# Performance work log

Measured on AMD Instinct MI355X. Metric: run time of the kernel, lower is better.

Reference implementation:

```python
import jax, jax.numpy as jnp
import numpy as np

B, S, D, H = 4, 2048, 1024, 16
HD = D // H


def setup_inputs() -> dict:
    key = jax.random.key(0)
    ks = jax.random.split(key, 12)
    def lin(k):
        return jax.random.normal(k, (D, D), dtype=jnp.float32) * 0.02
    return {
        "query": jax.random.normal(ks[0], (B, S, D), dtype=jnp.float32),
        "key": jax.random.normal(ks[1], (B, S, D), dtype=jnp.float32),
        "value": jax.random.normal(ks[2], (B, S, D), dtype=jnp.float32),
        "Wq": lin(ks[3]), "bq": jnp.zeros((D,), jnp.float32),
        "Wk": lin(ks[4]), "bk": jnp.zeros((D,), jnp.float32),
        "Wv": lin(ks[5]), "bv": jnp.zeros((D,), jnp.float32),
        "Wo": lin(ks[6]), "bo": jnp.zeros((D,), jnp.float32),
        "pad_mask": jnp.ones((B, S), dtype=jnp.int32),
    }


def reference(query, key, value, Wq, bq, Wk, bk, Wv, bv, Wo, bo, pad_mask):
    # torch nn.Linear convention: y = x @ W.T + b
    Q = query @ Wq.T + bq   # [B,Sq,D]
    K = key @ Wk.T + bk     # [B,Sk,D]
    V = value @ Wv.T + bv
    Sq, Sk = Q.shape[1], K.shape[1]
    Q = Q.reshape(B, Sq, H, HD).transpose(0, 2, 1, 3)  # [B,H,Sq,hd]
    K = K.reshape(B, Sk, H, HD).transpose(0, 2, 1, 3)
    V = V.reshape(B, Sk, H, HD).transpose(0, 2, 1, 3)
    scores = jnp.einsum('bhqd,bhkd->bhqk', Q, K) / jnp.sqrt(jnp.float32(HD))
    # causal (lookahead) mask
    causal = jnp.tril(jnp.ones((Sq, Sk), dtype=bool))
    scores = jnp.where(causal[None, None], scores, -jnp.inf)
    # pad mask broadcast [B,1,Sq,1]
    pm = (pad_mask[:, None, :, None] != 0)
    scores = jnp.where(pm, scores, -jnp.inf)
    attn = jax.nn.softmax(scores, axis=-1)
    out = jnp.einsum('bhqk,bhkd->bhqd', attn, V)  # [B,H,Sq,hd]
    out = out.transpose(0, 2, 1, 3).reshape(B, Sq, D)
    return out @ Wo.T + bo
```

## Files before the change

kernel.cpp:

```cpp
#include <hip/hip_runtime.h>
#include <hip/hip_bf16.h>
#include <stdint.h>

typedef __attribute__((ext_vector_type(8))) short bf16x8;
typedef __attribute__((ext_vector_type(4))) float f32x4;

#define HD 64
#define NH 16
#define SEQ 2048
#define DM 1024

#define GLDS16(gp, lp)                                                      \
    __builtin_amdgcn_global_load_lds(                                       \
        (const __attribute__((address_space(1))) void*)(gp),                \
        (__attribute__((address_space(3))) void*)(lp), 16, 0, 0)

__device__ __forceinline__ unsigned pk2(float lo, float hi) {
    union { unsigned u; __hip_bfloat16 h[2]; } w;
    w.h[0] = __float2bfloat16(lo);
    w.h[1] = __float2bfloat16(hi);
    return w.u;
}

__device__ inline bf16x8 cvt8(const float* __restrict__ p) {
    float4 a = *(const float4*)p;
    float4 b = *(const float4*)(p + 4);
    union { bf16x8 v; __hip_bfloat16 e[8]; } u;
    u.e[0] = __float2bfloat16(a.x); u.e[1] = __float2bfloat16(a.y);
    u.e[2] = __float2bfloat16(a.z); u.e[3] = __float2bfloat16(a.w);
    u.e[4] = __float2bfloat16(b.x); u.e[5] = __float2bfloat16(b.y);
    u.e[6] = __float2bfloat16(b.z); u.e[7] = __float2bfloat16(b.w);
    return u.v;
}

__global__ __launch_bounds__(256)
void cvtw(const float* __restrict__ a, const float* __restrict__ b,
          const float* __restrict__ c, const float* __restrict__ d,
          __hip_bfloat16* __restrict__ o)
{
    int g = blockIdx.x * 256 + threadIdx.x;
    int t = g * 4;
    const float* src;
    switch (t >> 20) {
        case 0: src = a; break;
        case 1: src = b; break;
        case 2: src = c; break;
        default: src = d; break;
    }
    float4 v = *(const float4*)(src + (t & 0xFFFFF));
    union { ushort4 u; __hip_bfloat16 e[4]; } w;
    w.e[0] = __float2bfloat16(v.x); w.e[1] = __float2bfloat16(v.y);
    w.e[2] = __float2bfloat16(v.z); w.e[3] = __float2bfloat16(v.w);
    *(ushort4*)(o + t) = w.u;
}

__device__ __forceinline__ bf16x8 ldfrag_f32(const char* base, int row, int quad) {
    f32x4 a = *(const f32x4*)(base + (size_t)row * 128 + (((2 * quad)     ^ (row & 7)) * 16));
    f32x4 b = *(const f32x4*)(base + (size_t)row * 128 + (((2 * quad + 1) ^ (row & 7)) * 16));
    union { bf16x8 v; unsigned u[4]; } w;
    w.u[0] = pk2(a[0], a[1]); w.u[1] = pk2(a[2], a[3]);
    w.u[2] = pk2(b[0], b[1]); w.u[3] = pk2(b[2], b[3]);
    return w.v;
}

__global__ __launch_bounds__(256, 4)
void qkvgemm(const float* __restrict__ Xq, const float* __restrict__ Xk,
             const float* __restrict__ Xv,
             const __hip_bfloat16* __restrict__ wb,
             const float* __restrict__ bq, const float* __restrict__ bk,
             const float* __restrict__ bv,
             __hip_bfloat16* __restrict__ Qh, __hip_bfloat16* __restrict__ Kh,
             __hip_bfloat16* __restrict__ Vt, float scaleQ)
{
    __shared__ alignas(16) float As[128 * 32];
    __shared__ alignas(16) __hip_bfloat16 Bs[128 * 32];

    const int tid  = threadIdx.x;
    const int lane = tid & 63;
    const int wv   = tid >> 6;
    const int quad = lane >> 4;
    const int l15  = lane & 15;
    const int wm   = (wv >> 1) * 64;
    const int wn   = (wv & 1) * 64;
    const int z    = blockIdx.z;

    const float* X = (z == 0) ? Xq : (z == 1) ? Xk : Xv;
    const __hip_bfloat16* W = wb + (size_t)z * (1024 * 1024);
    const float* bias = (z == 0) ? bq : (z == 1) ? bk : bv;

    int lin = blockIdx.y * 8 + blockIdx.x;
    const int bx = lin >> 6;
    const int by = ((lin & 7) << 3) | ((lin >> 3) & 7);
    const int m0 = by * 128;
    const int n0 = bx * 128;

    f32x4 acc[4][4] = {};

    for (int k0 = 0; k0 < 1024; k0 += 32) {
        #pragma unroll
        for (int it = 0; it < 4; ++it) {
            int g = tid + it * 256;
            int row = g >> 3, cl = (g & 7) ^ (row & 7);
            GLDS16(&X[(size_t)(m0 + row) * 1024 + k0 + cl * 4],
                   (char*)As + (size_t)g * 16);
        }
        #pragma unroll
        for (int it = 0; it < 2; ++it) {
            int c = tid + it * 256;
            int row = c >> 2, cg = c & 3;
            GLDS16(&W[(size_t)(n0 + row) * 1024 + k0 + cg * 8],
                   (char*)Bs + (size_t)c * 16);
        }
        __syncthreads();

        bf16x8 af[4], bfr[4];
        #pragma unroll
        for (int i = 0; i < 4; ++i)
            af[i] = ldfrag_f32((const char*)As, wm + i * 16 + l15, quad);
        #pragma unroll
        for (int j = 0; j < 4; ++j)
            bfr[j] = *(const bf16x8*)(&Bs[(wn + j * 16 + l15) * 32 + quad * 8]);

        #pragma unroll
        for (int i = 0; i < 4; ++i)
            #pragma unroll
            for (int j = 0; j < 4; ++j)
                acc[i][j] = __builtin_amdgcn_mfma_f32_16x16x32_bf16(
                    af[i], bfr[j], acc[i][j], 0, 0, 0);
        __syncthreads();
    }

    const float scale = (z == 0) ? scaleQ : 1.0f;
    #pragma unroll
    for (int j = 0; j < 4; ++j) {
        int n = n0 + wn + j * 16 + l15;
        float bv2 = bias[n];
        int h = n >> 6, hd = n & 63;
        #pragma unroll
        for (int i = 0; i < 4; ++i) {
            int mb = m0 + wm + i * 16 + quad * 4;
            if (z < 2) {
                __hip_bfloat16* Y = (z == 0) ? Qh : Kh;
                #pragma unroll
                for (int r = 0; r < 4; ++r) {
                    int m = mb + r;
                    int b = m >> 11, s = m & 2047;
                    Y[((size_t)(b * NH + h) * SEQ + s) * HD + hd] =
                        __float2bfloat16((acc[i][j][r] + bv2) * scale);
                }
            } else {
                int b = mb >> 11, s = mb & 2047;
                union { ushort4 u; __hip_bfloat16 e[4]; } w;
                #pragma unroll
                for (int r = 0; r < 4; ++r)
                    w.e[r] = __float2bfloat16(acc[i][j][r] + bv2);
                *(ushort4*)(&Vt[((size_t)(b * NH + h) * HD + hd) * SEQ + s]) = w.u;
            }
        }
    }
}

__global__ __launch_bounds__(256)
void ogemm(const __hip_bfloat16* __restrict__ X,
           const __hip_bfloat16* __restrict__ Wb,
           const float* __restrict__ bias,
           float* __restrict__ Y,
           int M, int N, int K)
{
    __shared__ alignas(16) __hip_bfloat16 As[128 * 32];
    __shared__ alignas(16) __hip_bfloat16 Bs[128 * 32];

    const int tid  = threadIdx.x;
    const int lane = tid & 63;
    const int wv   = tid >> 6;
    const int quad = lane >> 4;
    const int l15  = lane & 15;
    const int wm   = (wv >> 1) * 64;
    const int wn   = (wv & 1) * 64;

    int lin = blockIdx.y * 8 + blockIdx.x;
    const int bx = lin >> 6;
    const int by = ((lin & 7) << 3) | ((lin >> 3) & 7);
    const int m0 = by * 128;
    const int n0 = bx * 128;

    f32x4 acc[4][4] = {};

    for (int k0 = 0; k0 < K; k0 += 32) {
        #pragma unroll
        for (int it = 0; it < 2; ++it) {
            int c = tid + it * 256;
            int row = c >> 2, cg = c & 3;
            GLDS16(&X[(size_t)(m0 + row) * K + k0 + cg * 8],
                   (char*)As + (size_t)c * 16);
            GLDS16(&Wb[(size_t)(n0 + row) * K + k0 + cg * 8],
                   (char*)Bs + (size_t)c * 16);
        }
        __syncthreads();

        bf16x8 af[4], bfr[4];
        #pragma unroll
        for (int i = 0; i < 4; ++i)
            af[i] = *(const bf16x8*)(&As[(wm + i * 16 + l15) * 32 + quad * 8]);
        #pragma unroll
        for (int j = 0; j < 4; ++j)
            bfr[j] = *(const bf16x8*)(&Bs[(wn + j * 16 + l15) * 32 + quad * 8]);

        #pragma unroll
        for (int i = 0; i < 4; ++i)
            #pragma unroll
            for (int j = 0; j < 4; ++j)
                acc[i][j] = __builtin_amdgcn_mfma_f32_16x16x32_bf16(
                    af[i], bfr[j], acc[i][j], 0, 0, 0);
        __syncthreads();
    }

    #pragma unroll
    for (int j = 0; j < 4; ++j) {
        int n = n0 + wn + j * 16 + l15;
        float bv = bias[n];
        #pragma unroll
        for (int i = 0; i < 4; ++i) {
            int mb = m0 + wm + i * 16 + quad * 4;
            #pragma unroll
            for (int r = 0; r < 4; ++r)
                Y[(size_t)(mb + r) * N + n] = acc[i][j][r] + bv;
        }
    }
}

__device__ __forceinline__ void swap16(unsigned& a, unsigned& b) {
    asm("v_permlane16_swap_b32 %0, %1" : "+v"(a), "+v"(b));
}

__device__ __forceinline__ void attn_tile(
    const bf16x8 (&aqs)[2], f32x4 (&os)[4], f32x4& o5,
    const __hip_bfloat16* __restrict__ K_, const __hip_bfloat16* __restrict__ V_,
    const bf16x8 ones, int kv0, int qabs, bool diag,
    int quad, int l15, int sw, int qp)
{
    f32x4 sv[4];
    __builtin_amdgcn_s_setprio(1);
    #pragma unroll
    for (int jk = 0; jk < 4; ++jk) {
        f32x4 s = {};
        #pragma unroll
        for (int ks = 0; ks < 2; ++ks) {
            bf16x8 kf = *(const bf16x8*)(
                &K_[(jk * 16 + l15) * 64 + (((ks * 4 + quad) ^ sw) * 8)]);
            s = __builtin_amdgcn_mfma_f32_16x16x32_bf16(kf, aqs[ks], s, 0, 0, 0);
        }
        sv[jk] = s;
    }
    __builtin_amdgcn_s_setprio(0);
    unsigned P[4][2];
    #pragma unroll
    for (int jk = 0; jk < 4; ++jk) {
        int kvb = kv0 + jk * 16 + quad * 4;
        #pragma unroll
        for (int h = 0; h < 2; ++h) {
            float e0 = __builtin_amdgcn_exp2f(sv[jk][2 * h]);
            float e1 = __builtin_amdgcn_exp2f(sv[jk][2 * h + 1]);
            if (diag) {
                e0 = (kvb + 2 * h     <= qabs) ? e0 : 0.f;
                e1 = (kvb + 2 * h + 1 <= qabs) ? e1 : 0.f;
            }
            P[jk][h] = pk2(e0, e1);
        }
    }
    swap16(P[0][0], P[1][0]);
    swap16(P[0][1], P[1][1]);
    swap16(P[2][0], P[3][0]);
    swap16(P[2][1], P[3][1]);
    union { bf16x8 v; unsigned u[4]; } fa0, fa1;
    fa0.u[0] = P[0][0]; fa0.u[1] = P[0][1]; fa0.u[2] = P[1][0]; fa0.u[3] = P[1][1];
    fa1.u[0] = P[2][0]; fa1.u[1] = P[2][1]; fa1.u[2] = P[3][0]; fa1.u[3] = P[3][1];
    __builtin_amdgcn_s_setprio(1);
    #pragma unroll
    for (int jn = 0; jn < 4; ++jn) {
        bf16x8 vb0 = *(const bf16x8*)(
            &V_[(jn * 16 + l15) * 64 + ((qp ^ sw) * 8)]);
        bf16x8 vb1 = *(const bf16x8*)(
            &V_[(jn * 16 + l15) * 64 + (((4 + qp) ^ sw) * 8)]);
        os[jn] = __builtin_amdgcn_mfma_f32_16x16x32_bf16(fa0.v, vb0, os[jn], 0, 0, 0);
        os[jn] = __builtin_amdgcn_mfma_f32_16x16x32_bf16(fa1.v, vb1, os[jn], 0, 0, 0);
    }
    o5 = __builtin_amdgcn_mfma_f32_16x16x32_bf16(fa0.v, ones, o5, 0, 0, 0);
    o5 = __builtin_amdgcn_mfma_f32_16x16x32_bf16(fa1.v, ones, o5, 0, 0, 0);
    __builtin_amdgcn_s_setprio(0);
}

__global__ __launch_bounds__(256, 4)
void attn(const __hip_bfloat16* __restrict__ Qh,
          const __hip_bfloat16* __restrict__ Kh,
          const __hip_bfloat16* __restrict__ Vt,
          __hip_bfloat16* __restrict__ O)
{
    __shared__ alignas(16) __hip_bfloat16 Ks[2][64 * 64];
    __shared__ alignas(16) __hip_bfloat16 VsT[2][64 * 64];

    const int tid  = threadIdx.x;
    const int lane = tid & 63;
    const int wv   = tid >> 6;
    const int quad = lane >> 4;
    const int l15  = lane & 15;
    const int bh   = blockIdx.y;
    const int b    = bh >> 4;
    const int h    = bh & 15;
    const int p    = blockIdx.x;
    const int sa   = p;
    const int sb   = 31 - p;
    const int sw   = l15 & 7;
    const int qp   = ((quad & 1) << 1) | (quad >> 1);

    const __hip_bfloat16* Qp  = Qh + (size_t)bh * SEQ * HD;
    const __hip_bfloat16* Kp  = Kh + (size_t)bh * SEQ * HD;
    const __hip_bfloat16* Vtp = Vt + (size_t)bh * HD * SEQ;

    union { bf16x8 v; short e[8]; } onesu;
    #pragma unroll
    for (int i = 0; i < 8; ++i) onesu.e[i] = (short)0x3F80;
    const bf16x8 ones = onesu.v;

    bf16x8 aq[2][2];
    #pragma unroll
    for (int s = 0; s < 2; ++s) {
        int qb = (s ? sb : sa) * 64;
        #pragma unroll
        for (int ks = 0; ks < 2; ++ks)
            aq[s][ks] = *(const bf16x8*)(
                &Qp[(size_t)(qb + wv * 16 + l15) * HD + ks * 32 + quad * 8]);
    }

    f32x4 o[2][4] = {};
    f32x4 o5[2]   = {};

    const int srow = tid >> 3;
    const int scg  = (tid & 7) ^ (srow & 7);
    const __hip_bfloat16* kSrc = Kp + (size_t)srow * HD + scg * 8;
    const __hip_bfloat16* vSrc = Vtp + (size_t)srow * SEQ + scg * 8;
    char* kDst0 = (char*)Ks[0]  + tid * 16;
    char* vDst0 = (char*)VsT[0] + tid * 16;

    auto STAGE = [&](int bufi, int kv0) {
        size_t kadv = (size_t)kv0 * HD;
        int boff = bufi * 8192;
        GLDS16(kSrc + kadv,           kDst0 + boff);
        GLDS16(kSrc + kadv + 32 * HD, kDst0 + boff + 4096);
        GLDS16(vSrc + kv0,            vDst0 + boff);
        GLDS16(vSrc + kv0 + 32 * SEQ, vDst0 + boff + 4096);
    };

    const int nit = sa + sb + 2;

    STAGE(0, 0);

    for (int i = 0; i < nit; ++i) {
        __syncthreads();

        int ni = i + 1;
        if (ni < nit) {
            int t2 = (ni <= sb) ? ni : ni - sb - 1;
            STAGE(ni & 1, t2 * 64);
        }

        const int cb    = i & 1;
        const bool isB  = (i <= sb);
        const int t     = isB ? i : i - sb - 1;
        const int strip = isB ? sb : sa;
        const int kv0   = t * 64;
        const bool diag = (t == strip);
        const int qabs  = strip * 64 + wv * 16 + l15;

        const __hip_bfloat16* K_ = Ks[cb];
        const __hip_bfloat16* V_ = VsT[cb];

        if (isB)
            attn_tile(aq[1], o[1], o5[1], K_, V_, ones, kv0, qabs, diag, quad, l15, sw, qp);
        else
            attn_tile(aq[0], o[0], o5[0], K_, V_, ones, kv0, qabs, diag, quad, l15, sw, qp);
    }

    #pragma unroll
    for (int s = 0; s < 2; ++s) {
        int strip = s ? sb : sa;
        float inv[4];
        #pragma unroll
        for (int r = 0; r < 4; ++r)
            inv[r] = 1.0f / o5[s][r];
        #pragma unroll
        for (int jn = 0; jn < 4; ++jn) {
            #pragma unroll
            for (int r = 0; r < 4; ++r) {
                int q = strip * 64 + wv * 16 + quad * 4 + r;
                O[((size_t)(b * SEQ + q)) * DM + h * HD + jn * 16 + l15] =
                    __float2bfloat16(o[s][jn][r] * inv[r]);
            }
        }
    }
}

extern "C" void kernel_launch(void* const* d_in, const int* in_sizes, int n_in,
                              void* d_out, int out_size, void* d_ws, size_t ws_size,
                              hipStream_t stream)
{
    const float* query = (const float*)d_in[0];
    const float* key_  = (const float*)d_in[1];
    const float* value = (const float*)d_in[2];
    const float* Wq = (const float*)d_in[3];
    const float* bq = (const float*)d_in[4];
    const float* Wk = (const float*)d_in[5];
    const float* bk = (const float*)d_in[6];
    const float* Wv = (const float*)d_in[7];
    const float* bv = (const float*)d_in[8];
    const float* Wo = (const float*)d_in[9];
    const float* bo = (const float*)d_in[10];

    const size_t WSZ = (size_t)1024 * 1024;
    const size_t MAT = (size_t)8192 * 1024;
    __hip_bfloat16* wb = (__hip_bfloat16*)d_ws;
    __hip_bfloat16* Qh = wb + 4 * WSZ;
    __hip_bfloat16* Kh = Qh + MAT;
    __hip_bfloat16* Vt = Kh + MAT;
    __hip_bfloat16* Oa = Vt + MAT;
    float* out = (float*)d_out;

    const float SC = 0.18033688f;

    dim3 bb(256);
    cvtw<<<4096, bb, 0, stream>>>(Wq, Wk, Wv, Wo, wb);
    qkvgemm<<<dim3(8, 64, 3), bb, 0, stream>>>(query, key_, value, wb,
                                               bq, bk, bv, Qh, Kh, Vt, SC);
    attn<<<dim3(16, 64), bb, 0, stream>>>(Qh, Kh, Vt, Oa);
    ogemm<<<dim3(8, 64), bb, 0, stream>>>(Oa, wb + 3 * WSZ, bo, out, 8192, 1024, 1024);
}
```

Measured before the change: 350.6 us.

## Double-buffer LDS tiles in QKV and output projection GEMMs

Both projection GEMMs now use two LDS buffers. The next K-tile's global-to-LDS loads are issued right after the barrier, so they run while MFMA work proceeds on the current tile. This also removes one of the two barriers per iteration, and ogemm gets a launch-bounds occupancy hint of 4 blocks. The cost is doubled LDS per block, which may reduce resident blocks for qkvgemm; if the compiler conservatively waits on the LDS-DMA loads before the LDS reads, the overlap will not happen.

```diff
diff --git a/kernel.cpp b/kernel.cpp
--- a/kernel.cpp
+++ b/kernel.cpp
@@ -20,17 +20,6 @@
     w.h[0] = __float2bfloat16(lo);
     w.h[1] = __float2bfloat16(hi);
     return w.u;
-}
-
-__device__ inline bf16x8 cvt8(const float* __restrict__ p) {
-    float4 a = *(const float4*)p;
-    float4 b = *(const float4*)(p + 4);
-    union { bf16x8 v; __hip_bfloat16 e[8]; } u;
-    u.e[0] = __float2bfloat16(a.x); u.e[1] = __float2bfloat16(a.y);
-    u.e[2] = __float2bfloat16(a.z); u.e[3] = __float2bfloat16(a.w);
-    u.e[4] = __float2bfloat16(b.x); u.e[5] = __float2bfloat16(b.y);
-    u.e[6] = __float2bfloat16(b.z); u.e[7] = __float2bfloat16(b.w);
-    return u.v;
 }
 
 __global__ __launch_bounds__(256)
@@ -72,8 +61,8 @@
              __hip_bfloat16* __restrict__ Qh, __hip_bfloat16* __restrict__ Kh,
              __hip_bfloat16* __restrict__ Vt, float scaleQ)
 {
-    __shared__ alignas(16) float As[128 * 32];
-    __shared__ alignas(16) __hip_bfloat16 Bs[128 * 32];
+    __shared__ alignas(16) float As[2][128 * 32];
+    __shared__ alignas(16) __hip_bfloat16 Bs[2][128 * 32];
 
     const int tid  = threadIdx.x;
     const int lane = tid & 63;
@@ -96,30 +85,38 @@
 
     f32x4 acc[4][4] = {};
 
-    for (int k0 = 0; k0 < 1024; k0 += 32) {
+    auto STAGE = [&](int bufi, int k0) {
         #pragma unroll
         for (int it = 0; it < 4; ++it) {
             int g = tid + it * 256;
             int row = g >> 3, cl = (g & 7) ^ (row & 7);
             GLDS16(&X[(size_t)(m0 + row) * 1024 + k0 + cl * 4],
-                   (char*)As + (size_t)g * 16);
+                   (char*)As[bufi] + (size_t)g * 16);
         }
         #pragma unroll
         for (int it = 0; it < 2; ++it) {
             int c = tid + it * 256;
             int row = c >> 2, cg = c & 3;
             GLDS16(&W[(size_t)(n0 + row) * 1024 + k0 + cg * 8],
-                   (char*)Bs + (size_t)c * 16);
-        }
+                   (char*)Bs[bufi] + (size_t)c * 16);
+        }
+    };
+
+    STAGE(0, 0);
+
+    for (int k = 0; k < 32; ++k) {
         __syncthreads();
-
+        if (k + 1 < 32)
+            STAGE((k + 1) & 1, (k + 1) * 32);
+
+        const int cb = k & 1;
         bf16x8 af[4], bfr[4];
         #pragma unroll
         for (int i = 0; i < 4; ++i)
-            af[i] = ldfrag_f32((const char*)As, wm + i * 16 + l15, quad);
+            af[i] = ldfrag_f32((const char*)As[cb], wm + i * 16 + l15, quad);
         #pragma unroll
         for (int j = 0; j < 4; ++j)
-            bfr[j] = *(const bf16x8*)(&Bs[(wn + j * 16 + l15) * 32 + quad * 8]);
+            bfr[j] = *(const bf16x8*)(&Bs[cb][(wn + j * 16 + l15) * 32 + quad * 8]);
 
         #pragma unroll
         for (int i = 0; i < 4; ++i)
@@ -127,7 +124,6 @@
             for (int j = 0; j < 4; ++j)
                 acc[i][j] = __builtin_amdgcn_mfma_f32_16x16x32_bf16(
                     af[i], bfr[j], acc[i][j], 0, 0, 0);
-        __syncthreads();
     }
 
     const float scale = (z == 0) ? scaleQ : 1.0f;
@@ -160,15 +156,15 @@
     }
 }
 
-__global__ __launch_bounds__(256)
+__global__ __launch_bounds__(256, 4)
 void ogemm(const __hip_bfloat16* __restrict__ X,
            const __hip_bfloat16* __restrict__ Wb,
            const float* __restrict__ bias,
            float* __restrict__ Y,
            int M, int N, int K)
 {
-    __shared__ alignas(16) __hip_bfloat16 As[128 * 32];
-    __shared__ alignas(16) __hip_bfloat16 Bs[128 * 32];
+    __shared__ alignas(16) __hip_bfloat16 As[2][128 * 32];
+    __shared__ alignas(16) __hip_bfloat16 Bs[2][128 * 32];
 
     const int tid  = threadIdx.x;
     const int lane = tid & 63;
@@ -186,25 +182,34 @@
 
     f32x4 acc[4][4] = {};
 
-    for (int k0 = 0; k0 < K; k0 += 32) {
+    auto STAGE = [&](int bufi, int k0) {
         #pragma unroll
         for (int it = 0; it < 2; ++it) {
             int c = tid + it * 256;
             int row = c >> 2, cg = c & 3;
             GLDS16(&X[(size_t)(m0 + row) * K + k0 + cg * 8],
-                   (char*)As + (size_t)c * 16);
+                   (char*)As[bufi] + (size_t)c * 16);
             GLDS16(&Wb[(size_t)(n0 + row) * K + k0 + cg * 8],
-                   (char*)Bs + (size_t)c * 16);
-        }
+                   (char*)Bs[bufi] + (size_t)c * 16);
+        }
+    };
+
+    STAGE(0, 0);
+
+    const int nk = K >> 5;
+    for (int k = 0; k < nk; ++k) {
         __syncthreads();
-
+        if (k + 1 < nk)
+            STAGE((k + 1) & 1, (k + 1) * 32);
+
+        const int cb = k & 1;
         bf16x8 af[4], bfr[4];
         #pragma unroll
         for (int i = 0; i < 4; ++i)
-            af[i] = *(const bf16x8*)(&As[(wm + i * 16 + l15) * 32 + quad * 8]);
+            af[i] = *(const bf16x8*)(&As[cb][(wm + i * 16 + l15) * 32 + quad * 8]);
         #pragma unroll
         for (int j = 0; j < 4; ++j)
-            bfr[j] = *(const bf16x8*)(&Bs[(wn + j * 16 + l15) * 32 + quad * 8]);
+            bfr[j] = *(const bf16x8*)(&Bs[cb][(wn + j * 16 + l15) * 32 + quad * 8]);
 
         #pragma unroll
         for (int i = 0; i < 4; ++i)
@@ -212,7 +217,6 @@
             for (int j = 0; j < 4; ++j)
                 acc[i][j] = __builtin_amdgcn_mfma_f32_16x16x32_bf16(
                     af[i], bfr[j], acc[i][j], 0, 0, 0);
-        __syncthreads();
     }
 
     #pragma unroll
```

Measured after the change: 363.7 us. +3.7%, slower.
